# Kernel tuning notes

Measured on AMD Instinct MI355X. Metric: run time of the kernel, lower is better.

## Reference

```python
import jax, jax.numpy as jnp
import numpy as np

IMG = 128                  # img_size
FMM = 35.0
SENSOR = 32.0
FUV = FMM * IMG / SENSOR   # focal length in pixels (screen space, in_ndc=False)
N_PTS = 16384
CHUNK = 1024               # points per scan step
R_SIL = 0.008              # silhouette pass radius (NDC)
R_DEP = 0.012              # depth pass radius (NDC)
K_SIL = 8
K_DEP = 16
DIST = 1.2


def _look_at(dist, elev_deg, azim_deg):
    # PyTorch3D look_at_view_transform with at=origin, up=+Y, degrees=True
    elev = jnp.deg2rad(elev_deg)
    azim = jnp.deg2rad(azim_deg)
    cam = jnp.stack([dist * jnp.cos(elev) * jnp.sin(azim),
                     dist * jnp.sin(elev),
                     dist * jnp.cos(elev) * jnp.cos(azim)], axis=-1)  # (B,3)
    up = jnp.array([0.0, 1.0, 0.0], dtype=cam.dtype)
    z_ax = -cam / (jnp.linalg.norm(cam, axis=-1, keepdims=True) + 1e-8)
    x_ax = jnp.cross(jnp.broadcast_to(up, z_ax.shape), z_ax)
    x_ax = x_ax / (jnp.linalg.norm(x_ax, axis=-1, keepdims=True) + 1e-8)
    y_ax = jnp.cross(z_ax, x_ax)
    R = jnp.stack([x_ax, y_ax, z_ax], axis=-1)   # columns are camera axes
    T = -jnp.einsum('bi,bij->bj', cam, R)        # X_cam = X_world @ R + T
    return R, T


def _project(pts, R, T):
    # world -> camera (row-vector convention) -> screen px -> PyTorch3D NDC
    Xc = jnp.einsum('bni,bij->bnj', pts, R) + T[:, None, :]
    z = Xc[..., 2]
    z_safe = jnp.where(z > 1e-5, z, 1.0)  # points behind camera are culled anyway
    xs = FUV * Xc[..., 0] / z_safe + IMG / 2.0
    ys = FUV * Xc[..., 1] / z_safe + IMG / 2.0
    x_ndc = 1.0 - 2.0 * xs / IMG
    y_ndc = 1.0 - 2.0 * ys / IMG
    return jnp.stack([x_ndc, y_ndc], axis=-1), z


def _rasterize(xy, z, r2, K):
    """Per-pixel K nearest-in-depth points within per-point NDC radius.
    xy: (B,N,2) NDC, z: (B,N) camera depth, r2: (B,N) squared radius.
    Returns zbuf, dists of shape (B,IMG,IMG,K), -1 for empty slots."""
    B, N, _ = xy.shape
    P = IMG * IMG
    # pixel-center NDC grid (PyTorch3D: +X left, +Y up; row-major flatten)
    gxs = 1.0 - (2.0 * jnp.arange(IMG, dtype=xy.dtype) + 1.0) / IMG  # per column
    gys = 1.0 - (2.0 * jnp.arange(IMG, dtype=xy.dtype) + 1.0) / IMG  # per row
    gx = jnp.tile(gxs, IMG)          # (P,)
    gy = jnp.repeat(gys, IMG)        # (P,)

    nch = N // CHUNK
    px = xy[..., 0].reshape(B, nch, CHUNK).swapaxes(0, 1)
    py = xy[..., 1].reshape(B, nch, CHUNK).swapaxes(0, 1)
    pz = z.reshape(B, nch, CHUNK).swapaxes(0, 1)
    pr2 = r2.reshape(B, nch, CHUNK).swapaxes(0, 1)

    def body(carry, c):
        top_z, top_d = carry
        cx, cy, cz, cr2 = c                               # each (B,CHUNK)
        dx = gx[None, :, None] - cx[:, None, :]           # (B,P,CHUNK)
        dy = gy[None, :, None] - cy[:, None, :]
        d2 = dx * dx + dy * dy
        ok = (d2 < cr2[:, None, :]) & (cz[:, None, :] > 0.0)
        zc = jnp.where(ok, cz[:, None, :], jnp.inf)
        cand_z = jnp.concatenate([top_z, zc], axis=-1)    # (B,P,K+CHUNK)
        cand_d = jnp.concatenate([top_d, d2], axis=-1)
        negz, idx = jax.lax.top_k(-cand_z, K)             # K smallest depths
        return (-negz, jnp.take_along_axis(cand_d, idx, axis=-1)), None

    init = (jnp.full((B, P, K), jnp.inf, dtype=xy.dtype),
            jnp.zeros((B, P, K), dtype=xy.dtype))
    (top_z, top_d), _ = jax.lax.scan(jax.checkpoint(body), init, (px, py, pz, pr2))
    valid = jnp.isfinite(top_z)
    zbuf = jnp.where(valid, top_z, -1.0).reshape(B, IMG, IMG, K)
    dists = jnp.where(valid, top_d, -1.0).reshape(B, IMG, IMG, K)
    return zbuf, dists


def setup_inputs() -> dict:
    key = jax.random.key(0)
    k1, k2 = jax.random.split(key)
    point_cloud = jax.random.normal(k1, (2, N_PTS, 6), dtype=jnp.float32) * 0.25
    param = jax.random.normal(k2, (2, 8, 3), dtype=jnp.float32) * 20.0  # degrees
    return {"point_cloud": point_cloud, "param": param}


def reference(point_cloud, param):
    pts = point_cloud[..., :3]
    B = pts.shape[0]
    elev0 = param[:, 1, 0]
    azim0 = param[:, 0, 0]

    # ---- silhouette pass (radius 0.008, K=8) + alpha compositing ----
    R0, T0 = _look_at(DIST, elev0, azim0)
    xy0, z0 = _project(pts, R0, T0)
    r2_sil = jnp.full((B, N_PTS), R_SIL * R_SIL, dtype=pts.dtype)
    _, dists_s = _rasterize(xy0, z0, r2_sil, K_SIL)
    alphas = jnp.where(dists_s >= 0.0, 1.0 - dists_s / (R_SIL * R_SIL), 0.0)
    trans = jnp.cumprod(1.0 - alphas, axis=-1)
    trans_excl = jnp.concatenate([jnp.ones_like(trans[..., :1]), trans[..., :-1]], axis=-1)
    sihlt_map = jnp.sum(alphas * trans_excl, axis=-1, keepdims=True) * 255.0  # (B,H,W,1)

    # ---- depth pass with random view (radius 0.012, K=16) ----
    kd = jax.random.key(42)
    ke, ka = jax.random.split(kd)
    elev_d = jax.random.uniform(ke, (B,), dtype=pts.dtype) * 60.0 - 30.0
    azim_d = jax.random.uniform(ka, (B,), dtype=pts.dtype) * 300.0 + azim0 + 30.0
    Rd, Td = _look_at(DIST, elev_d, azim_d)
    xyd, zd = _project(pts, Rd, Td)
    r2_dep = jnp.full((B, N_PTS), R_DEP * R_DEP, dtype=pts.dtype)
    zbuf_d, _ = _rasterize(xyd, zd, r2_dep, K_DEP)
    depth_ini = zbuf_d[..., 0]

    # density-aware adaptive radius (detached, per source .detach())
    area = jnp.sum((jax.lax.stop_gradient(depth_ini) > 0.0).astype(pts.dtype), axis=(1, 2))
    pa_radius = area / 16384.0 * 0.057                      # (B,)
    r2_ada = jnp.broadcast_to((pa_radius * pa_radius)[:, None], (B, N_PTS))

    zbuf_a, dists_a = _rasterize(xyd, zd, r2_ada, K_DEP)
    depth_img = zbuf_a[..., :8]
    dist_top = dists_a[..., :8]
    return (sihlt_map, depth_img, dist_top)
```

## Files before the change

kernel.cpp:

```cpp
#include <hip/hip_runtime.h>
#include <hip/hip_cooperative_groups.h>
#include <cstring>
#include <cstdint>

namespace cg = cooperative_groups;

#define NPTS 16384
#define FUVC 140.0f
#define R_SILF 0.008f
#define R_DEPF 0.012f
#define R2_SIL (0.008f*0.008f)
#define R2_DEP (0.012f*0.012f)
#define CH 512

#define AREA_OFF  48
#define PA_OFF    50
#define R2ADA_OFF 52
#define TICK0     54
#define TICK1     55
#define CNT_SIL   64
#define OFF_SIL   2112
#define CNT_ADA   4160
#define OFF_ADA   6208
#define FLAGS8    8256
#define FLAGS     8256
#define ZERO_END  16448
#define PROJ0     41024
#define PROJ1     172096
#define LSILF     303168
#define LADAF     827456
#define WS1_WORDS 2007104u
#define WS1_NEEDED ((size_t)WS1_WORDS * 4u)
#define LSIL      303168
#define LADA      434240
#define WS2_WORDS 729152u
#define WS2_NEEDED ((size_t)WS2_WORDS * 4u)

#define FUSED_BLOCKS 1024
#define FUSED_NT (FUSED_BLOCKS * 256)

__device__ __forceinline__ void cam_calc(float elev, float azim, float c[12]) {
    const float D2R = 0.017453292519943295f;
    float er = elev * D2R, ar = azim * D2R;
    float ce = cosf(er), se = sinf(er), ca = cosf(ar), sa = sinf(ar);
    float cx = 1.2f * ce * sa, cy = 1.2f * se, cz = 1.2f * ce * ca;
    float n = sqrtf(cx*cx + cy*cy + cz*cz) + 1e-8f;
    float zx = -cx / n, zy = -cy / n, zz = -cz / n;
    float xx = zz, xy = 0.0f, xz = -zx;
    float xn = sqrtf(xx*xx + xy*xy + xz*xz) + 1e-8f;
    xx /= xn; xz /= xn;
    float yx = zy*xz - zz*xy, yy = zz*xx - zx*xz, yz = zx*xy - zy*xx;
    c[0]=xx; c[1]=xy; c[2]=xz; c[3]=yx; c[4]=yy; c[5]=yz;
    c[6]=zx; c[7]=zy; c[8]=zz;
    c[9]  = -(cx*xx + cy*xy + cz*xz);
    c[10] = -(cx*yx + cy*yy + cz*yz);
    c[11] = -(cx*zx + cy*zy + cz*zz);
}

__device__ __forceinline__ void cam_compute(const float* __restrict__ param,
                                            float* __restrict__ ws,
                                            int t, float ue0, float ue1,
                                            float ua0, float ua1) {
    int b = t >> 1, cam = t & 1;
    float azim0 = param[b * 24 + 0];
    float elev0 = param[b * 24 + 3];
    float elev, azim;
    if (cam == 0) { elev = elev0; azim = azim0; }
    else {
        float ue = b ? ue1 : ue0;
        float ua = b ? ua1 : ua0;
        elev = ue * 60.0f - 30.0f;
        azim = ua * 300.0f + azim0 + 30.0f;
    }
    float c[12];
    cam_calc(elev, azim, c);
    float* w = ws + t * 12;
    #pragma unroll
    for (int i = 0; i < 12; i++) w[i] = c[i];
}

__device__ __forceinline__ float4 project_pt(const float* __restrict__ P,
                                             const float c[12]) {
    float X = P[0], Y = P[1], Z = P[2];
    float xc = X*c[0] + Y*c[1] + Z*c[2] + c[9];
    float yc = X*c[3] + Y*c[4] + Z*c[5] + c[10];
    float zc = X*c[6] + Y*c[7] + Z*c[8] + c[11];
    float zs = zc > 1e-5f ? zc : 1.0f;
    float px = 1.0f - (FUVC * xc / zs + 64.0f) * (1.0f/64.0f);
    float py = 1.0f - (FUVC * yc / zs + 64.0f) * (1.0f/64.0f);
    return make_float4(px, py, zc, 0.0f);
}

// ... 53 lines not shown
        bool take = oz[7 - k] < tz[k];
        mz[k] = take ? oz[7 - k] : tz[k];
        md[k] = take ? od[7 - k] : td[k];
    }
    CE8(0,4) CE8(1,5) CE8(2,6) CE8(3,7)
    CE8(0,2) CE8(1,3) CE8(4,6) CE8(5,7)
    CE8(0,1) CE8(2,3) CE8(4,5) CE8(6,7)
    #pragma unroll
    for (int k = 0; k < 8; k++) { tz[k] = mz[k]; td[k] = md[k]; }
}

__device__ __forceinline__ void merge_seq8(float tz[8], float td[8],
                                           const float* __restrict__ ozp,
                                           const float* __restrict__ odp) {
    float mz[8], md[8];
    #pragma unroll
    for (int k = 0; k < 8; k++) {
        float oz = ozp[7 - k], od = odp[7 - k];
        bool take = oz < tz[k];
        mz[k] = take ? oz : tz[k];
        md[k] = take ? od : td[k];
    }
    CE8(0,4) CE8(1,5) CE8(2,6) CE8(3,7)
    CE8(0,2) CE8(1,3) CE8(4,6) CE8(5,7)
    CE8(0,1) CE8(2,3) CE8(4,5) CE8(6,7)
    #pragma unroll
    for (int k = 0; k < 8; k++) { tz[k] = mz[k]; td[k] = md[k]; }
}

__device__ __forceinline__ void scan1024(unsigned* uw, unsigned cbase,
                                         unsigned obase, unsigned* s, int t) {
    unsigned c0 = uw[cbase + t*4 + 0];
    unsigned c1 = uw[cbase + t*4 + 1];
    unsigned c2 = uw[cbase + t*4 + 2];
    unsigned c3 = uw[cbase + t*4 + 3];
    unsigned tot = c0 + c1 + c2 + c3;
    s[t] = tot; __syncthreads();
    for (int off = 1; off < 256; off <<= 1) {
        unsigned v = (t >= off) ? s[t - off] : 0u;
        __syncthreads();
        s[t] += v;
        __syncthreads();
    }
    unsigned base = s[t] - tot;
    uw[obase + t*4 + 0] = base;
    uw[obase + t*4 + 1] = base + c0;
    uw[obase + t*4 + 2] = base + c0 + c1;
    uw[obase + t*4 + 3] = base + c0 + c1 + c2;
    uw[cbase + t*4 + 0] = 0;
    uw[cbase + t*4 + 1] = 0;
    uw[cbase + t*4 + 2] = 0;
    uw[cbase + t*4 + 3] = 0;
}

__device__ __forceinline__ void body_area_scan(float* __restrict__ ws, int job,
                                               int t, unsigned* s) {
    unsigned* uw = (unsigned*)ws;
    if (job < 2) {
        int b = job;
        unsigned acc = 0;
        #pragma unroll
        for (int j = 0; j < 16; j++) {
            unsigned w = uw[FLAGS8 + b * 4096 + t * 16 + j];
            acc += __popc(w & 0x01010101u);
        }
        s[t] = acc; __syncthreads();
        for (int off = 128; off > 0; off >>= 1) {
            if (t < off) s[t] += s[t + off];
            __syncthreads();
        }
        if (t == 0) {
            unsigned area = s[0];
            uw[AREA_OFF + b] = area;
            float pa = (float)area * (1.0f/16384.0f) * 0.057f;
            ws[PA_OFF + b] = pa;
            ws[R2ADA_OFF + b] = pa * pa;
        }
    } else {
        int b = job - 2;
        scan1024(uw, CNT_SIL + b * 1024, OFF_SIL + b * 1024, s, t);
    }
}

__device__ __forceinline__ void body_cnt_ada(float* __restrict__ ws, int p) {
    unsigned* uw = (unsigned*)ws;
    int b = p >> 14;
    float4 q = ((const float4*)(ws + PROJ1))[p];
    float pa = ws[PA_OFF + b];
    int bxl, bxh, byl, byh;
    bin_bbox(q, pa, bxl, bxh, byl, byh);
    for (int by = byl; by <= byh; by++)
        for (int bx = bxl; bx <= bxh; bx++)
            atomicAdd(&uw[CNT_ADA + b * 1024 + by * 32 + bx], 1u);
}

__device__ __forceinline__ void body_scat_sil(float* __restrict__ ws, int p) {
    unsigned* uw = (unsigned*)ws;
    int b = p >> 14;
    float4 q = ((const float4*)(ws + PROJ0))[p];
    int bxl, bxh, byl, byh;
    bin_bbox(q, R_SILF, bxl, bxh, byl, byh);
    for (int by = byl; by <= byh; by++)
        for (int bx = bxl; bx <= bxh; bx++) {
            unsigned bin = b * 1024 + by * 32 + bx;
            unsigned idx = uw[OFF_SIL + bin] + atomicAdd(&uw[CNT_SIL + bin], 1u);
            ((float4*)(ws + LSILF))[b * 65536 + idx] = q;
// ... 25 lines not shown
    int b = p >> 14;
    float4 q = ((const float4*)(ws + PROJ1))[p];
    float pa = ws[PA_OFF + b];
    int bxl, bxh, byl, byh;
    bin_bbox(q, pa, bxl, bxh, byl, byh);
    for (int by = byl; by <= byh; by++)
        for (int bx = bxl; bx <= bxh; bx++) {
            unsigned bin = b * 1024 + by * 32 + bx;
            unsigned idx = uw[OFF_ADA + bin] + atomicAdd(&uw[CNT_ADA + bin], 1u);
            ((float4*)(ws + LADAF))[b * 147456 + idx] = q;
        }
}

__device__ __forceinline__ void body_gather256(const float* __restrict__ ws,
                                               float* __restrict__ out,
                                               int id, int t,
                                               float* __restrict__ sm) {
    const unsigned* uw = (const unsigned*)ws;
    bool sil = id < 2048;
    int gt = sil ? id : id - 2048;
    int b = gt >> 10;
    int tile = gt & 1023;
    int p = t & 15, seg = t >> 4;
    int bx = tile & 31, by = tile >> 5;
    int col = (bx << 2) + (p & 3), row = (by << 2) + (p >> 2);
    float gx = 1.0f - (float)(2*col + 1) * (1.0f/128.0f);
    float gy = 1.0f - (float)(2*row + 1) * (1.0f/128.0f);
    float r2 = sil ? R2_SIL : ws[R2ADA_OFF + b];
    unsigned start = sil ? uw[OFF_SIL + b * 1024 + tile] : uw[OFF_ADA + b * 1024 + tile];
    unsigned len   = sil ? uw[CNT_SIL + b * 1024 + tile] : uw[CNT_ADA + b * 1024 + tile];
    const float4* lst = sil ? ((const float4*)(ws + LSILF)) + b * 65536 + start
                            : ((const float4*)(ws + LADAF)) + b * 147456 + start;

    float tz[8], td[8];
    #pragma unroll
    for (int k = 0; k < 8; k++) { tz[k] = INFINITY; td[k] = 0.0f; }

    unsigned i = (unsigned)seg;
    while (i + 112 < len) {
        float4 cb[8];
        #pragma unroll
        for (int u = 0; u < 8; u++) cb[u] = lst[i + 16u * (unsigned)u];
        #pragma unroll
        for (int u = 0; u < 8; u++) hit_test(cb[u], gx, gy, r2, tz, td);
        i += 128;
    }
    for (; i < len; i += 16) hit_test(lst[i], gx, gy, r2, tz, td);

    merge_sorted8(tz, td, 16);
    merge_sorted8(tz, td, 32);

    int w = t >> 6;
    if ((t & 63) < 16) {
        float* dst = sm + (w * 16 + p) * 16;
        #pragma unroll
        for (int k = 0; k < 8; k++) { dst[k] = tz[k]; dst[8 + k] = td[k]; }
    }
    __syncthreads();
    if (t < 16) {
        #pragma unroll
        for (int ww = 1; ww < 4; ww++) {
            const float* src = sm + (ww * 16 + p) * 16;
            merge_seq8(tz, td, src, src + 8);
        }
        int pix = (b << 14) + row * 128 + col;
        if (sil) {
            float trans = 1.0f, acc = 0.0f;
            #pragma unroll
            for (int k = 0; k < 8; k++) {
                float a = (tz[k] != INFINITY) ? (1.0f - td[k] / R2_SIL) : 0.0f;
                acc += a * trans;
                trans *= (1.0f - a);
            }
            out[pix] = acc * 255.0f;
        } else {
            float* dep = out + 32768  + (size_t)pix * 8;
            float* dst = out + 294912 + (size_t)pix * 8;
            #pragma unroll
            for (int k = 0; k < 8; k++) {
                bool v = (tz[k] != INFINITY);
                dep[k] = v ? tz[k] : -1.0f;
                dst[k] = v ? td[k] : -1.0f;
            }
        }
    }
}

__device__ __forceinline__ void body_gather(const float* __restrict__ ws,
                                            float* __restrict__ out,
                                            int id, int lane) {
    const unsigned* uw = (const unsigned*)ws;
    bool sil = id < 2048;
    int gt = sil ? id : id - 2048;
    int b = gt >> 10;
    int tile = gt & 1023;
    int p = lane & 15, s = lane >> 4;
    int bx = tile & 31, by = tile >> 5;
    int col = (bx << 2) + (p & 3), row = (by << 2) + (p >> 2);
    float gx = 1.0f - (float)(2*col + 1) * (1.0f/128.0f);
    float gy = 1.0f - (float)(2*row + 1) * (1.0f/128.0f);
    float r2 = sil ? R2_SIL : ws[R2ADA_OFF + b];
    unsigned start = sil ? uw[OFF_SIL + b * 1024 + tile] : uw[OFF_ADA + b * 1024 + tile];
    unsigned len   = sil ? uw[CNT_SIL + b * 1024 + tile] : uw[CNT_ADA + b * 1024 + tile];
    const float4* lst = sil ? ((const float4*)(ws + LSILF)) + b * 65536 + start
                            : ((const float4*)(ws + LADAF)) + b * 147456 + start;

    float tz[8], td[8];
    #pragma unroll
    for (int k = 0; k < 8; k++) { tz[k] = INFINITY; td[k] = 0.0f; }

    unsigned i = (unsigned)s;
    while (i + 28 < len) {
        float4 cb[8];
        #pragma unroll
        for (int u = 0; u < 8; u++) cb[u] = lst[i + 4u * (unsigned)u];
        #pragma unroll
        for (int u = 0; u < 8; u++) hit_test(cb[u], gx, gy, r2, tz, td);
        i += 32;
    }
    for (; i < len; i += 4) hit_test(lst[i], gx, gy, r2, tz, td);

    merge_sorted8(tz, td, 16);
    merge_sorted8(tz, td, 32);

    if (s == 0) {
        int pix = (b << 14) + row * 128 + col;
        if (sil) {
            float trans = 1.0f, acc = 0.0f;
            #pragma unroll
            for (int k = 0; k < 8; k++) {
                float a = (tz[k] != INFINITY) ? (1.0f - td[k] / R2_SIL) : 0.0f;
                acc += a * trans;
                trans *= (1.0f - a);
            }
            out[pix] = acc * 255.0f;
        } else {
            float* dep = out + 32768  + (size_t)pix * 8;
            float* dst = out + 294912 + (size_t)pix * 8;
            #pragma unroll
            for (int k = 0; k < 8; k++) {
                bool v = (tz[k] != INFINITY);
                dep[k] = v ? tz[k] : -1.0f;
                dst[k] = v ? td[k] : -1.0f;
            }
        }
    }
}

__global__ __launch_bounds__(256) void k_fusedp(const float* __restrict__ pc,
                                                const float* __restrict__ param,
                                                float* __restrict__ ws,
                                                float* __restrict__ out,
                                                float ue0, float ue1,
                                                float ua0, float ua1) {
    cg::grid_group grid = cg::this_grid();
    unsigned* uw = (unsigned*)ws;
    __shared__ unsigned sh[2048];
    __shared__ unsigned shLast;
    int t = threadIdx.x;
    int tid = blockIdx.x * 256 + t;

    for (int i = 48 + tid; i < ZERO_END; i += FUSED_NT) uw[i] = 0u;
    if (tid < 4) cam_compute(param, ws, tid, ue0, ue1, ua0, ua1);
    grid.sync();

    if (blockIdx.x < 128) {
        int b = blockIdx.x >> 6;
        int p = ((blockIdx.x & 63) << 8) + t;
        unsigned char* fb = (unsigned char*)(uw + FLAGS8);
        const float* P = pc + ((size_t)b * NPTS + p) * 6;
        float c0[12], c1[12];
        const float* w0 = ws + (b * 2) * 12;
        #pragma unroll
        for (int i = 0; i < 12; i++) { c0[i] = w0[i]; c1[i] = w0[12 + i]; }

        #pragma unroll
        for (int j = 0; j < 4; j++) sh[t * 4 + j] = 0u;
        __syncthreads();

        float4 q0 = project_pt(P, c0);
        ((float4*)(ws + PROJ0))[b * NPTS + p] = q0;
        int bxl, bxh, byl, byh;
        bin_bbox(q0, R_SILF, bxl, bxh, byl, byh);
        for (int by = byl; by <= byh; by++)
            for (int bx = bxl; bx <= bxh; bx++)
                atomicAdd(&sh[by * 32 + bx], 1u);

        float4 q1 = project_pt(P, c1);
        ((float4*)(ws + PROJ1))[b * NPTS + p] = q1;
        if (q1.z > 0.0f) {
            int cl, chh, rl, rh;
            pix_range(q1.x, R_DEPF, cl, chh);
            pix_range(q1.y, R_DEPF, rl, rh);
            for (int rr = rl; rr <= rh; rr++) {
                float gyv = 1.0f - (float)(2 * rr + 1) * (1.0f/128.0f);
                float dy = gyv - q1.y;
                for (int cc = cl; cc <= chh; cc++) {
                    float gxv = 1.0f - (float)(2 * cc + 1) * (1.0f/128.0f);
                    float dx = gxv - q1.x;
                    if (dx*dx + dy*dy < R2_DEP) fb[b * NPTS + rr * 128 + cc] = 1;
                }
            }
        }
        __syncthreads();
        #pragma unroll
        for (int j = 0; j < 4; j++) {
            unsigned c = sh[t * 4 + j];
            if (c) atomicAdd(&uw[CNT_SIL + b * 1024 + t * 4 + j], c);
        }
        __threadfence();
    }
    if (t == 0) shLast = (atomicAdd(&uw[TICK0], 1u) == FUSED_BLOCKS - 1) ? 1u : 0u;
    __syncthreads();
    if (shLast) {
        __threadfence();
        for (int job = 0; job < 4; job++) {
            body_area_scan(ws, job, t, sh);
            __syncthreads();
        }
        __threadfence();
    }
    grid.sync();

    if (blockIdx.x < 128) {
        int b = blockIdx.x >> 6;
        int p = ((blockIdx.x & 63) << 8) + t;
        float4 q = ((const float4*)(ws + PROJ1))[b * NPTS + p];
        float pa = ws[PA_OFF + b];
        #pragma unroll
        for (int j = 0; j < 4; j++) sh[t * 4 + j] = 0u;
        __syncthreads();
        int bxl, bxh, byl, byh;
        bin_bbox(q, pa, bxl, bxh, byl, byh);
        for (int by = byl; by <= byh; by++)
            for (int bx = bxl; bx <= bxh; bx++)
                atomicAdd(&sh[by * 32 + bx], 1u);
        __syncthreads();
        #pragma unroll
        for (int j = 0; j < 4; j++) {
            unsigned c = sh[t * 4 + j];
            if (c) atomicAdd(&uw[CNT_ADA + b * 1024 + t * 4 + j], c);
        }
        __threadfence();
    } else if (blockIdx.x < 256) {
        int blk = blockIdx.x - 128;
        int b = blk >> 6;
        int p = ((blk & 63) << 8) + t;
        float4 q = ((const float4*)(ws + PROJ0))[b * NPTS + p];
        int bxl, bxh, byl, byh;
        bin_bbox(q, R_SILF, bxl, bxh, byl, byh);
        #pragma unroll
        for (int j = 0; j < 4; j++) sh[t * 4 + j] = 0u;
        __syncthreads();
        for (int by = byl; by <= byh; by++)
            for (int bx = bxl; bx <= bxh; bx++)
                atomicAdd(&sh[by * 32 + bx], 1u);
        __syncthreads();
        #pragma unroll
        for (int j = 0; j < 4; j++) {
            int bin = t * 4 + j;
            unsigned c = sh[bin];
            unsigned gb = 0;
            if (c) gb = uw[OFF_SIL + b * 1024 + bin] +
                        atomicAdd(&uw[CNT_SIL + b * 1024 + bin], c);
            sh[1024 + bin] = gb;
            sh[bin] = 0u;
        }
        __syncthreads();
        for (int by = byl; by <= byh; by++)
            for (int bx = bxl; bx <= bxh; bx++) {
                int bin = by * 32 + bx;
                unsigned loc = atomicAdd(&sh[bin], 1u);
                ((float4*)(ws + LSILF))[b * 65536 + sh[1024 + bin] + loc] = q;
            }
        __threadfence();
    }
    if (t == 0) shLast = (atomicAdd(&uw[TICK1], 1u) == FUSED_BLOCKS - 1) ? 1u : 0u;
    __syncthreads();
    if (shLast) {
        __threadfence();
        if (t < 128) body_scan_ada(ws, t >> 6, t & 63);
        __threadfence();
    }
    grid.sync();

    if (blockIdx.x < 128) {
        int b = blockIdx.x >> 6;
        int p = ((blockIdx.x & 63) << 8) + t;
        float4 q = ((const float4*)(ws + PROJ1))[b * NPTS + p];
        float pa = ws[PA_OFF + b];
        int bxl, bxh, byl, byh;
        bin_bbox(q, pa, bxl, bxh, byl, byh);
        #pragma unroll
        for (int j = 0; j < 4; j++) sh[t * 4 + j] = 0u;
        __syncthreads();
        for (int by = byl; by <= byh; by++)
            for (int bx = bxl; bx <= bxh; bx++)
                atomicAdd(&sh[by * 32 + bx], 1u);
        __syncthreads();
        #pragma unroll
        for (int j = 0; j < 4; j++) {
            int bin = t * 4 + j;
            unsigned c = sh[bin];
            unsigned gb = 0;
            if (c) gb = uw[OFF_ADA + b * 1024 + bin] +
                        atomicAdd(&uw[CNT_ADA + b * 1024 + bin], c);
            sh[1024 + bin] = gb;
            sh[bin] = 0u;
        }
        __syncthreads();
        for (int by = byl; by <= byh; by++)
            for (int bx = bxl; bx <= bxh; bx++) {
                int bin = by * 32 + bx;
                unsigned loc = atomicAdd(&sh[bin], 1u);
                ((float4*)(ws + LADAF))[b * 147456 + sh[1024 + bin] + loc] = q;
            }
    }
    grid.sync();

    for (int rep = 0; rep < 4; rep++) {
        int id = rep * 1024 + blockIdx.x;
        body_gather256(ws, out, id, t, (float*)sh);
        __syncthreads();
    }
}


__global__ __launch_bounds__(256) void k_zero(float* __restrict__ ws) {
    unsigned* uw = (unsigned*)ws;
    int gid = blockIdx.x * 256 + threadIdx.x;
    int stride = gridDim.x * 256;
    for (int i = 48 + gid; i < ZERO_END; i += stride) uw[i] = 0u;
}

__global__ __launch_bounds__(256) void k_proj_v3(const float* __restrict__ pc,
                                                 const float* __restrict__ param,
                                                 float* __restrict__ ws,
                                                 float ue0, float ue1,
                                                 float ua0, float ua1) {
    int b = blockIdx.x >> 6;
    int p = ((blockIdx.x & 63) << 8) + threadIdx.x;
    float azim0 = param[b * 24 + 0];
    float elev0 = param[b * 24 + 3];
    float c0[12], c1[12];
    cam_calc(elev0, azim0, c0);
    float ue = b ? ue1 : ue0;
    float ua = b ? ua1 : ua0;
    cam_calc(ue * 60.0f - 30.0f, ua * 300.0f + azim0 + 30.0f, c1);

    unsigned* uw = (unsigned*)ws;
    unsigned char* fb = (unsigned char*)(uw + FLAGS8);
    const float* P = pc + ((size_t)b * NPTS + p) * 6;

    float4 q0 = project_pt(P, c0);
    ((float4*)(ws + PROJ0))[b * NPTS + p] = q0;
    int bxl, bxh, byl, byh;
    bin_bbox(q0, R_SILF, bxl, bxh, byl, byh);
    for (int by = byl; by <= byh; by++)
        for (int bx = bxl; bx <= bxh; bx++)
            atomicAdd(&uw[CNT_SIL + b * 1024 + by * 32 + bx], 1u);

    float4 q1 = project_pt(P, c1);
    ((float4*)(ws + PROJ1))[b * NPTS + p] = q1;
    if (q1.z > 0.0f) {
        int cl, chh, rl, rh;
        pix_range(q1.x, R_DEPF, cl, chh);
        pix_range(q1.y, R_DEPF, rl, rh);
        for (int rr = rl; rr <= rh; rr++) {
            float gy = 1.0f - (float)(2 * rr + 1) * (1.0f/128.0f);
            float dy = gy - q1.y;
            for (int cc = cl; cc <= chh; cc++) {
                float gx = 1.0f - (float)(2 * cc + 1) * (1.0f/128.0f);
                float dx = gx - q1.x;
                if (dx*dx + dy*dy < R2_DEP) fb[b * NPTS + rr * 128 + cc] = 1;
            }
        }
    }
}

__global__ __launch_bounds__(256) void k_area_scan_v3(float* __restrict__ ws) {
    __shared__ unsigned s[256];
    body_area_scan(ws, blockIdx.x, threadIdx.x, s);
}

__global__ __launch_bounds__(64) void k_cntada_scatsil(float* __restrict__ ws) {
    int id = blockIdx.x;
    bool isCnt = id < 512;
    int p = ((isCnt ? id : id - 512) << 6) + threadIdx.x;
    if (isCnt) body_cnt_ada(ws, p);
    else       body_scat_sil(ws, p);
}

__global__ __launch_bounds__(64) void k_scan_ada64(float* __restrict__ ws) {
    body_scan_ada(ws, blockIdx.x, threadIdx.x);
}

__global__ __launch_bounds__(64) void k_scatter_ada_v2(float* __restrict__ ws) {
    body_scat_ada(ws, (blockIdx.x << 6) + threadIdx.x);
}

__global__ __launch_bounds__(256) void k_gather_v4(const float* __restrict__ ws,
                                                   float* __restrict__ out) {
    __shared__ float sm[1024];
    body_gather256(ws, out, blockIdx.x, threadIdx.x, sm);
}


__global__ __launch_bounds__(256) void k_init(const float* __restrict__ param,
                                              float* __restrict__ ws,
                                              float ue0, float ue1,
                                              float ua0, float ua1) {
    unsigned* uw = (unsigned*)ws;
    int gid = blockIdx.x * 256 + threadIdx.x;
    int stride = gridDim.x * 256;
    for (int i = gid; i < 2048; i += stride) { uw[CNT_SIL + i] = 0u; uw[CNT_ADA + i] = 0u; }
    for (int i = gid; i < 32768; i += stride) uw[FLAGS + i] = 0u;
    if (gid < 2) uw[AREA_OFF + gid] = 0u;
    if (gid < 4) cam_compute(param, ws, gid, ue0, ue1, ua0, ua1);
}

__global__ __launch_bounds__(256) void k_proj_count(const float* __restrict__ pc,
                                                    float* __restrict__ ws) {
    unsigned* uw = (unsigned*)ws;
    int b = blockIdx.x >> 6;
    int p = ((blockIdx.x & 63) << 8) + threadIdx.x;
    const float* P = pc + ((size_t)b * NPTS + p) * 6;
    float c0[12], c1[12];
    const float* w0 = ws + (b * 2) * 12;
    #pragma unroll
    for (int i = 0; i < 12; i++) { c0[i] = w0[i]; c1[i] = w0[12 + i]; }

    float4 q0 = project_pt(P, c0);
    ((float4*)(ws + PROJ0))[b * NPTS + p] = q0;
    int bxl, bxh, byl, byh;
    bin_bbox(q0, R_SILF, bxl, bxh, byl, byh);
    for (int by = byl; by <= byh; by++)
        for (int bx = bxl; bx <= bxh; bx++)
            atomicAdd(&uw[CNT_SIL + b * 1024 + by * 32 + bx], 1u);

    float4 q1 = project_pt(P, c1);
    ((float4*)(ws + PROJ1))[b * NPTS + p] = q1;
    if (q1.z > 0.0f) {
        int cl, chh, rl, rh;
        pix_range(q1.x, R_DEPF, cl, chh);
        pix_range(q1.y, R_DEPF, rl, rh);
        for (int rr = rl; rr <= rh; rr++) {
            float gy = 1.0f - (float)(2 * rr + 1) * (1.0f/128.0f);
            float dy = gy - q1.y;
            for (int cc = cl; cc <= chh; cc++) {
                float gx = 1.0f - (float)(2 * cc + 1) * (1.0f/128.0f);
                float dx = gx - q1.x;
                if (dx*dx + dy*dy < R2_DEP) uw[FLAGS + b * NPTS + rr * 128 + cc] = 1u;
            }
        }
    }
}
// ... 236 lines not shown
    #pragma unroll
    for (int k = 0; k < 8; k++) {
        bool v = (tz[k] != INFINITY);
        dep[k] = v ? tz[k] : -1.0f;
        dst[k] = v ? td[k] : -1.0f;
    }
}

static inline uint32_t rotl32(uint32_t x, int r) { return (x << r) | (x >> (32 - r)); }

static void tf2x32(uint32_t k0, uint32_t k1, uint32_t c0, uint32_t c1,
                   uint32_t* o0, uint32_t* o1) {
    uint32_t ks0 = k0, ks1 = k1, ks2 = k0 ^ k1 ^ 0x1BD11BDAu;
    uint32_t x0 = c0 + ks0, x1 = c1 + ks1;
    static const int rA[4] = {13, 15, 26, 6};
    static const int rB[4] = {17, 29, 16, 24};
    #define RND4(R) do { for (int i = 0; i < 4; i++) { x0 += x1; x1 = rotl32(x1, R[i]); x1 ^= x0; } } while (0)
    RND4(rA); x0 += ks1; x1 += ks2 + 1u;
    RND4(rB); x0 += ks2; x1 += ks0 + 2u;
    RND4(rA); x0 += ks0; x1 += ks1 + 3u;
    RND4(rB); x0 += ks1; x1 += ks2 + 4u;
    RND4(rA); x0 += ks2; x1 += ks0 + 5u;
    #undef RND4
    *o0 = x0; *o1 = x1;
}

static inline float bits_to_unit_float(uint32_t bits) {
    uint32_t fb = (bits >> 9) | 0x3f800000u;
    float f;
    memcpy(&f, &fb, 4);
    return f - 1.0f;
}

extern "C" void kernel_launch(void* const* d_in, const int* in_sizes, int n_in,
                              void* d_out, int out_size, void* d_ws, size_t ws_size,
                              hipStream_t stream) {
    const float* pc    = (const float*)d_in[0];
    const float* param = (const float*)d_in[1];
    float* out = (float*)d_out;
    float* ws  = (float*)d_ws;

    uint32_t ke0, ke1, ka0, ka1, b1, b2;
    tf2x32(0u, 42u, 0u, 0u, &ke0, &ke1);
    tf2x32(0u, 42u, 0u, 1u, &ka0, &ka1);
    float ue[2], ua[2];
    for (uint32_t i = 0; i < 2; i++) {
        tf2x32(ke0, ke1, 0u, i, &b1, &b2);
        ue[i] = bits_to_unit_float(b1 ^ b2);
        tf2x32(ka0, ka1, 0u, i, &b1, &b2);
        ua[i] = bits_to_unit_float(b1 ^ b2);
    }
    float ue0 = ue[0], ue1 = ue[1], ua0 = ua[0], ua1 = ua[1];

    if (ws_size >= WS1_NEEDED) {
        int dev = 0;
        hipGetDevice(&dev);
        hipDeviceProp_t prop;
        bool coop = (hipGetDeviceProperties(&prop, dev) == hipSuccess) &&
                    prop.cooperativeLaunch;
        if (coop) {
            int maxB = 0;
            if (hipOccupancyMaxActiveBlocksPerMultiprocessor(&maxB, k_fusedp, 256, 0)
                    != hipSuccess ||
                maxB * prop.multiProcessorCount < FUSED_BLOCKS)
                coop = false;
        }
        if (coop) {
            void* args[] = { (void*)&pc, (void*)&param, (void*)&ws, (void*)&out,
                             (void*)&ue0, (void*)&ue1, (void*)&ua0, (void*)&ua1 };
            hipError_t e = hipLaunchCooperativeKernel((const void*)k_fusedp,
                                                      dim3(FUSED_BLOCKS), dim3(256),
                                                      args, 0, stream);
            if (e == hipSuccess) return;
        }
        k_zero          <<<16, 256, 0, stream>>>(ws);
        k_proj_v3       <<<128, 256, 0, stream>>>(pc, param, ws, ue0, ue1, ua0, ua1);
        k_area_scan_v3  <<<4, 256, 0, stream>>>(ws);
        k_cntada_scatsil<<<1024, 64, 0, stream>>>(ws);
        k_scan_ada64    <<<2, 64, 0, stream>>>(ws);
        k_scatter_ada_v2<<<512, 64, 0, stream>>>(ws);
        k_gather_v4     <<<4096, 256, 0, stream>>>(ws, out);
    } else if (ws_size >= WS2_NEEDED) {
        k_init      <<<64, 256, 0, stream>>>(param, ws, ue0, ue1, ua0, ua1);
        k_proj_count<<<128, 256, 0, stream>>>(pc, ws);
        k_area_scan <<<4, 256, 0, stream>>>(ws);
        k_count_ada <<<128, 256, 0, stream>>>(ws);
        k_scan_ada  <<<2, 256, 0, stream>>>(ws);
        k_scatter   <<<128, 256, 0, stream>>>(ws);
        k_gather_sil<<<128, 256, 0, stream>>>(ws, out);
        k_gather_ada<<<128, 256, 0, stream>>>(ws, out);
    } else {
        cam_kernel_fb<<<1, 64, 0, stream>>>(param, ws, ue0, ue1, ua0, ua1);
        raster_AB<<<256, 256, 0, stream>>>(pc, ws, out);
        raster_C <<<128, 256, 0, stream>>>(pc, ws, out);
    }
}
```

Measured before the change: 85.72 us.

## Restructure cooperative kernel to three grid syncs with per-block histograms

Replaces the cooperative fused kernel with a version that drops the initial zeroing and camera grid sync. Each block computes its camera inline and writes non-atomic per-block histograms and coverage bitmaps to workspace, and the adaptive list is binned by a conservative maximum radius so its counts can be computed before the area is known. Separate blocks then perform reductions and scans, which removes the last-block ticket logic and one full counting pass. The change needs more workspace, and the larger adaptive bins add candidate points to the gather. Shared-memory merge rows are padded to 17 floats to avoid bank conflicts.

```diff
diff --git a/kernel.cpp b/kernel.cpp
--- a/kernel.cpp
+++ b/kernel.cpp
@@ -9,6 +9,7 @@
 #define FUVC 140.0f
 #define R_SILF 0.008f
 #define R_DEPF 0.012f
+#define R_ADA_MAXF 0.057f
 #define R2_SIL (0.008f*0.008f)
 #define R2_DEP (0.012f*0.012f)
 #define CH 512
@@ -16,8 +17,6 @@
 #define AREA_OFF  48
 #define PA_OFF    50
 #define R2ADA_OFF 52
-#define TICK0     54
-#define TICK1     55
 #define CNT_SIL   64
 #define OFF_SIL   2112
 #define CNT_ADA   4160
@@ -35,9 +34,17 @@
 #define LADA      434240
 #define WS2_WORDS 729152u
 #define WS2_NEEDED ((size_t)WS2_WORDS * 4u)
+#define HSIL      2007104u
+#define HADA      2138176u
+#define BMAP      2269248u
+#define OFFA_SIL  2334784u
+#define OFFB_SIL  2336834u
+#define OFFA_ADA  2338882u
+#define OFFB_ADA  2340932u
+#define WS0_WORDS 2342980u
+#define WS0_NEEDED ((size_t)WS0_WORDS * 4u)
 
 #define FUSED_BLOCKS 1024
-#define FUSED_NT (FUSED_BLOCKS * 256)
 
 __device__ __forceinline__ void cam_calc(float elev, float azim, float c[12]) {
     const float D2R = 0.017453292519943295f;
@@ -197,6 +204,297 @@
     uw[cbase + t*4 + 2] = 0;
     uw[cbase + t*4 + 3] = 0;
 }
+
+__device__ __forceinline__ void job_scan64(unsigned* __restrict__ uw,
+                                           unsigned histBase, unsigned offaBase,
+                                           unsigned offbBase, unsigned* s, int t) {
+    unsigned c[4];
+    #pragma unroll
+    for (int j = 0; j < 4; j++) {
+        int bin = t * 4 + j;
+        unsigned acc = 0;
+        for (int blk = 0; blk < 64; blk++)
+            acc += uw[histBase + blk * 1024 + bin];
+        c[j] = acc;
+    }
+    unsigned tot = c[0] + c[1] + c[2] + c[3];
+    s[t] = tot; __syncthreads();
+    for (int off = 1; off < 256; off <<= 1) {
+        unsigned v = (t >= off) ? s[t - off] : 0u;
+        __syncthreads();
+        s[t] += v;
+        __syncthreads();
+    }
+    unsigned run = s[t] - tot;
+    #pragma unroll
+    for (int j = 0; j < 4; j++) {
+        uw[offaBase + t * 4 + j] = run;
+        uw[offbBase + t * 4 + j] = run;
+        run += c[j];
+    }
+    if (t == 255) uw[offaBase + 1024] = s[255];
+}
+
+__device__ __forceinline__ void job_area64(float* __restrict__ ws,
+                                           unsigned bmapBase, int b,
+                                           unsigned* s, int t) {
+    unsigned* uw = (unsigned*)ws;
+    unsigned acc = 0;
+    #pragma unroll
+    for (int w = 0; w < 2; w++) {
+        int word = t * 2 + w;
+        unsigned orv = 0;
+        for (int blk = 0; blk < 64; blk++)
+            orv |= uw[bmapBase + blk * 512 + word];
+        acc += __popc(orv);
+    }
+    s[t] = acc; __syncthreads();
+    for (int off = 128; off > 0; off >>= 1) {
+        if (t < off) s[t] += s[t + off];
+        __syncthreads();
+    }
+    if (t == 0) {
+        float pa = (float)s[0] * (1.0f/16384.0f) * 0.057f;
+        ws[R2ADA_OFF + b] = pa * pa;
+    }
+}
+
+__device__ __forceinline__ void body_gather256v2(const float* __restrict__ ws,
+                                                 float* __restrict__ out,
+                                                 int id, int t,
+                                                 float* __restrict__ sm) {
+    const unsigned* uw = (const unsigned*)ws;
+    bool sil = id < 2048;
+    int gt = sil ? id : id - 2048;
+    int b = gt >> 10;
+    int tile = gt & 1023;
+    int p = t & 15, seg = t >> 4;
+    int bx = tile & 31, by = tile >> 5;
+    int col = (bx << 2) + (p & 3), row = (by << 2) + (p >> 2);
+    float gx = 1.0f - (float)(2*col + 1) * (1.0f/128.0f);
+    float gy = 1.0f - (float)(2*row + 1) * (1.0f/128.0f);
+    float r2 = sil ? R2_SIL : ws[R2ADA_OFF + b];
+    unsigned offa = sil ? (OFFA_SIL + b * 1025 + tile) : (OFFA_ADA + b * 1025 + tile);
+    unsigned start = uw[offa];
+    unsigned len   = uw[offa + 1] - start;
+    const float4* lst = sil ? ((const float4*)(ws + LSILF)) + b * 65536 + start
+                            : ((const float4*)(ws + LADAF)) + b * 147456 + start;
+
+    float tz[8], td[8];
+    #pragma unroll
+    for (int k = 0; k < 8; k++) { tz[k] = INFINITY; td[k] = 0.0f; }
+
+    unsigned i = (unsigned)seg;
+    while (i + 112 < len) {
+        float4 cb[8];
+        #pragma unroll
+        for (int u = 0; u < 8; u++) cb[u] = lst[i + 16u * (unsigned)u];
+        #pragma unroll
+        for (int u = 0; u < 8; u++) hit_test(cb[u], gx, gy, r2, tz, td);
+        i += 128;
+    }
+    for (; i < len; i += 16) hit_test(lst[i], gx, gy, r2, tz, td);
+
+    merge_sorted8(tz, td, 16);
+    merge_sorted8(tz, td, 32);
+
+    int w = t >> 6;
+    if ((t & 63) < 16) {
+        float* dst = sm + (w * 16 + p) * 17;
+        #pragma unroll
+        for (int k = 0; k < 8; k++) { dst[k] = tz[k]; dst[8 + k] = td[k]; }
+    }
+    __syncthreads();
+    if (t < 16) {
+        #pragma unroll
+        for (int ww = 1; ww < 4; ww++) {
+            const float* src = sm + (ww * 16 + p) * 17;
+            merge_seq8(tz, td, src, src + 8);
+        }
+        int pix = (b << 14) + row * 128 + col;
+        if (sil) {
+            float trans = 1.0f, acc = 0.0f;
+            #pragma unroll
+            for (int k = 0; k < 8; k++) {
+                float a = (tz[k] != INFINITY) ? (1.0f - td[k] / R2_SIL) : 0.0f;
+                acc += a * trans;
+                trans *= (1.0f - a);
+            }
+            out[pix] = acc * 255.0f;
+        } else {
+            float* dep = out + 32768  + (size_t)pix * 8;
+            float* dst = out + 294912 + (size_t)pix * 8;
+            #pragma unroll
+            for (int k = 0; k < 8; k++) {
+                bool v = (tz[k] != INFINITY);
+                dep[k] = v ? tz[k] : -1.0f;
+                dst[k] = v ? td[k] : -1.0f;
+            }
+        }
+    }
+}
+
+__global__ __launch_bounds__(256) void k_fused3(const float* __restrict__ pc,
+                                                const float* __restrict__ param,
+                                                float* __restrict__ ws,
+                                                float* __restrict__ out,
+                                                float ue0, float ue1,
+                                                float ua0, float ua1) {
+    cg::grid_group grid = cg::this_grid();
+    unsigned* uw = (unsigned*)ws;
+    __shared__ unsigned sh[2048];
+    int t = threadIdx.x;
+    int blk = blockIdx.x;
+
+    if (blk < 128) {
+        int b = blk >> 6;
+        int p = ((blk & 63) << 8) + t;
+        float azim0 = param[b * 24 + 0];
+        float elev0 = param[b * 24 + 3];
+        float c0[12];
+        cam_calc(elev0, azim0, c0);
+        #pragma unroll
+        for (int j = 0; j < 4; j++) sh[t * 4 + j] = 0u;
+        __syncthreads();
+        float4 q0 = project_pt(pc + ((size_t)b * NPTS + p) * 6, c0);
+        ((float4*)(ws + PROJ0))[b * NPTS + p] = q0;
+        int bxl, bxh, byl, byh;
+        bin_bbox(q0, R_SILF, bxl, bxh, byl, byh);
+        for (int by = byl; by <= byh; by++)
+            for (int bx = bxl; bx <= bxh; bx++)
+                atomicAdd(&sh[by * 32 + bx], 1u);
+        __syncthreads();
+        #pragma unroll
+        for (int j = 0; j < 4; j++)
+            uw[HSIL + blk * 1024 + t * 4 + j] = sh[t * 4 + j];
+    } else if (blk < 256) {
+        int blk2 = blk - 128;
+        int b = blk2 >> 6;
+        int p = ((blk2 & 63) << 8) + t;
+        float azim0 = param[b * 24 + 0];
+        float ue = b ? ue1 : ue0;
+        float ua = b ? ua1 : ua0;
+        float c1[12];
+        cam_calc(ue * 60.0f - 30.0f, ua * 300.0f + azim0 + 30.0f, c1);
+        #pragma unroll
+        for (int j = 0; j < 4; j++) sh[t * 4 + j] = 0u;
+        sh[1024 + t * 2 + 0] = 0u;
+        sh[1024 + t * 2 + 1] = 0u;
+        __syncthreads();
+        float4 q1 = project_pt(pc + ((size_t)b * NPTS + p) * 6, c1);
+        ((float4*)(ws + PROJ1))[b * NPTS + p] = q1;
+        if (q1.z > 0.0f) {
+            int cl, chh, rl, rh;
+            pix_range(q1.x, R_DEPF, cl, chh);
+            pix_range(q1.y, R_DEPF, rl, rh);
+            for (int rr = rl; rr <= rh; rr++) {
+                float gyv = 1.0f - (float)(2 * rr + 1) * (1.0f/128.0f);
+                float dy = gyv - q1.y;
+                for (int cc = cl; cc <= chh; cc++) {
+                    float gxv = 1.0f - (float)(2 * cc + 1) * (1.0f/128.0f);
+                    float dx = gxv - q1.x;
+                    if (dx*dx + dy*dy < R2_DEP) {
+                        int pix = rr * 128 + cc;
+                        atomicOr(&sh[1024 + (pix >> 5)], 1u << (pix & 31));
+                    }
+                }
+            }
+        }
+        int bxl, bxh, byl, byh;
+        bin_bbox(q1, R_ADA_MAXF, bxl, bxh, byl, byh);
+        for (int by = byl; by <= byh; by++)
+            for (int bx = bxl; bx <= bxh; bx++)
+                atomicAdd(&sh[by * 32 + bx], 1u);
+        __syncthreads();
+        #pragma unroll
+        for (int j = 0; j < 4; j++)
+            uw[HADA + blk2 * 1024 + t * 4 + j] = sh[t * 4 + j];
+        uw[BMAP + blk2 * 512 + t * 2 + 0] = sh[1024 + t * 2 + 0];
+        uw[BMAP + blk2 * 512 + t * 2 + 1] = sh[1024 + t * 2 + 1];
+    }
+    grid.sync();
+
+    if (blk < 2) {
+        job_scan64(uw, HSIL + blk * 65536, OFFA_SIL + blk * 1025,
+                   OFFB_SIL + blk * 1024, sh, t);
+    } else if (blk < 4) {
+        int b = blk - 2;
+        job_scan64(uw, HADA + b * 65536, OFFA_ADA + b * 1025,
+                   OFFB_ADA + b * 1024, sh, t);
+    } else if (blk < 6) {
+        int b = blk - 4;
+        job_area64(ws, BMAP + b * 32768, b, sh, t);
+    }
+    grid.sync();
+
+    if (blk < 128) {
+        int b = blk >> 6;
+        int p = ((blk & 63) << 8) + t;
+        float4 q = ((const float4*)(ws + PROJ0))[b * NPTS + p];
+        int bxl, bxh, byl, byh;
+        bin_bbox(q, R_SILF, bxl, bxh, byl, byh);
+        #pragma unroll
+        for (int j = 0; j < 4; j++) sh[t * 4 + j] = 0u;
+        __syncthreads();
+        for (int by = byl; by <= byh; by++)
+            for (int bx = bxl; bx <= bxh; bx++)
+                atomicAdd(&sh[by * 32 + bx], 1u);
+        __syncthreads();
+        #pragma unroll
+        for (int j = 0; j < 4; j++) {
+            int bin = t * 4 + j;
+            unsigned c = sh[bin];
+            unsigned gb = 0;
+            if (c) gb = atomicAdd(&uw[OFFB_SIL + b * 1024 + bin], c);
+            sh[1024 + bin] = gb;
+            sh[bin] = 0u;
+        }
+        __syncthreads();
+        for (int by = byl; by <= byh; by++)
+            for (int bx = bxl; bx <= bxh; bx++) {
+                int bin = by * 32 + bx;
+                unsigned loc = atomicAdd(&sh[bin], 1u);
+                ((float4*)(ws + LSILF))[b * 65536 + sh[1024 + bin] + loc] = q;
+            }
+    } else if (blk < 256) {
+        int blk2 = blk - 128;
+        int b = blk2 >> 6;
+        int p = ((blk2 & 63) << 8) + t;
+        float4 q = ((const float4*)(ws + PROJ1))[b * NPTS + p];
+        int bxl, bxh, byl, byh;
+        bin_bbox(q, R_ADA_MAXF, bxl, bxh, byl, byh);
+        #pragma unroll
+        for (int j = 0; j < 4; j++) sh[t * 4 + j] = 0u;
+        __syncthreads();
+        for (int by = byl; by <= byh; by++)
+            for (int bx = bxl; bx <= bxh; bx++)
+                atomicAdd(&sh[by * 32 + bx], 1u);
+        __syncthreads();
+        #pragma unroll
+        for (int j = 0; j < 4; j++) {
+            int bin = t * 4 + j;
+            unsigned c = sh[bin];
+            unsigned gb = 0;
+            if (c) gb = atomicAdd(&uw[OFFB_ADA + b * 1024 + bin], c);
+            sh[1024 + bin] = gb;
+            sh[bin] = 0u;
+        }
+        __syncthreads();
+        for (int by = byl; by <= byh; by++)
+            for (int bx = bxl; bx <= bxh; bx++) {
+                int bin = by * 32 + bx;
+                unsigned loc = atomicAdd(&sh[bin], 1u);
+                ((float4*)(ws + LADAF))[b * 147456 + sh[1024 + bin] + loc] = q;
+            }
+    }
+    grid.sync();
+
+    for (int rep = 0; rep < 4; rep++) {
+        body_gather256v2(ws, out, rep * 1024 + blk, t, (float*)sh);
+        __syncthreads();
+    }
+}
+
 
 __device__ __forceinline__ void body_area_scan(float* __restrict__ ws, int job,
                                                int t, unsigned* s) {
@@ -328,7 +626,7 @@
 
     int w = t >> 6;
     if ((t & 63) < 16) {
-        float* dst = sm + (w * 16 + p) * 16;
+        float* dst = sm + (w * 16 + p) * 17;
         #pragma unroll
         for (int k = 0; k < 8; k++) { dst[k] = tz[k]; dst[8 + k] = td[k]; }
     }
@@ -336,7 +634,7 @@
     if (t < 16) {
         #pragma unroll
         for (int ww = 1; ww < 4; ww++) {
-            const float* src = sm + (ww * 16 + p) * 16;
+            const float* src = sm + (ww * 16 + p) * 17;
             merge_seq8(tz, td, src, src + 8);
         }
         int pix = (b << 14) + row * 128 + col;
@@ -362,246 +660,6 @@
     }
 }
 
-__device__ __forceinline__ void body_gather(const float* __restrict__ ws,
-                                            float* __restrict__ out,
-                                            int id, int lane) {
-    const unsigned* uw = (const unsigned*)ws;
-    bool sil = id < 2048;
-    int gt = sil ? id : id - 2048;
-    int b = gt >> 10;
-    int tile = gt & 1023;
-    int p = lane & 15, s = lane >> 4;
-    int bx = tile & 31, by = tile >> 5;
-    int col = (bx << 2) + (p & 3), row = (by << 2) + (p >> 2);
-    float gx = 1.0f - (float)(2*col + 1) * (1.0f/128.0f);
-    float gy = 1.0f - (float)(2*row + 1) * (1.0f/128.0f);
-    float r2 = sil ? R2_SIL : ws[R2ADA_OFF + b];
-    unsigned start = sil ? uw[OFF_SIL + b * 1024 + tile] : uw[OFF_ADA + b * 1024 + tile];
-    unsigned len   = sil ? uw[CNT_SIL + b * 1024 + tile] : uw[CNT_ADA + b * 1024 + tile];
-    const float4* lst = sil ? ((const float4*)(ws + LSILF)) + b * 65536 + start
-                            : ((const float4*)(ws + LADAF)) + b * 147456 + start;
-
-    float tz[8], td[8];
-    #pragma unroll
-    for (int k = 0; k < 8; k++) { tz[k] = INFINITY; td[k] = 0.0f; }
-
-    unsigned i = (unsigned)s;
-    while (i + 28 < len) {
-        float4 cb[8];
-        #pragma unroll
-        for (int u = 0; u < 8; u++) cb[u] = lst[i + 4u * (unsigned)u];
-        #pragma unroll
-        for (int u = 0; u < 8; u++) hit_test(cb[u], gx, gy, r2, tz, td);
-        i += 32;
-    }
-    for (; i < len; i += 4) hit_test(lst[i], gx, gy, r2, tz, td);
-
-    merge_sorted8(tz, td, 16);
-    merge_sorted8(tz, td, 32);
-
-    if (s == 0) {
-        int pix = (b << 14) + row * 128 + col;
-        if (sil) {
-            float trans = 1.0f, acc = 0.0f;
-            #pragma unroll
-            for (int k = 0; k < 8; k++) {
-                float a = (tz[k] != INFINITY) ? (1.0f - td[k] / R2_SIL) : 0.0f;
-                acc += a * trans;
-                trans *= (1.0f - a);
-            }
-            out[pix] = acc * 255.0f;
-        } else {
-            float* dep = out + 32768  + (size_t)pix * 8;
-            float* dst = out + 294912 + (size_t)pix * 8;
-            #pragma unroll
-            for (int k = 0; k < 8; k++) {
-                bool v = (tz[k] != INFINITY);
-                dep[k] = v ? tz[k] : -1.0f;
-                dst[k] = v ? td[k] : -1.0f;
-            }
-        }
-    }
-}
-
-__global__ __launch_bounds__(256) void k_fusedp(const float* __restrict__ pc,
-                                                const float* __restrict__ param,
-                                                float* __restrict__ ws,
-                                                float* __restrict__ out,
-                                                float ue0, float ue1,
-                                                float ua0, float ua1) {
-    cg::grid_group grid = cg::this_grid();
-    unsigned* uw = (unsigned*)ws;
-    __shared__ unsigned sh[2048];
-    __shared__ unsigned shLast;
-    int t = threadIdx.x;
-    int tid = blockIdx.x * 256 + t;
-
-    for (int i = 48 + tid; i < ZERO_END; i += FUSED_NT) uw[i] = 0u;
-    if (tid < 4) cam_compute(param, ws, tid, ue0, ue1, ua0, ua1);
-    grid.sync();
-
-    if (blockIdx.x < 128) {
-        int b = blockIdx.x >> 6;
-        int p = ((blockIdx.x & 63) << 8) + t;
-        unsigned char* fb = (unsigned char*)(uw + FLAGS8);
-        const float* P = pc + ((size_t)b * NPTS + p) * 6;
-        float c0[12], c1[12];
-        const float* w0 = ws + (b * 2) * 12;
-        #pragma unroll
-        for (int i = 0; i < 12; i++) { c0[i] = w0[i]; c1[i] = w0[12 + i]; }
-
-        #pragma unroll
-        for (int j = 0; j < 4; j++) sh[t * 4 + j] = 0u;
-        __syncthreads();
-
-        float4 q0 = project_pt(P, c0);
-        ((float4*)(ws + PROJ0))[b * NPTS + p] = q0;
-        int bxl, bxh, byl, byh;
-        bin_bbox(q0, R_SILF, bxl, bxh, byl, byh);
-        for (int by = byl; by <= byh; by++)
-            for (int bx = bxl; bx <= bxh; bx++)
-                atomicAdd(&sh[by * 32 + bx], 1u);
-
-        float4 q1 = project_pt(P, c1);
-        ((float4*)(ws + PROJ1))[b * NPTS + p] = q1;
-        if (q1.z > 0.0f) {
-            int cl, chh, rl, rh;
-            pix_range(q1.x, R_DEPF, cl, chh);
-            pix_range(q1.y, R_DEPF, rl, rh);
-            for (int rr = rl; rr <= rh; rr++) {
-                float gyv = 1.0f - (float)(2 * rr + 1) * (1.0f/128.0f);
-                float dy = gyv - q1.y;
-                for (int cc = cl; cc <= chh; cc++) {
-                    float gxv = 1.0f - (float)(2 * cc + 1) * (1.0f/128.0f);
-                    float dx = gxv - q1.x;
-                    if (dx*dx + dy*dy < R2_DEP) fb[b * NPTS + rr * 128 + cc] = 1;
-                }
-            }
-        }
-        __syncthreads();
-        #pragma unroll
-        for (int j = 0; j < 4; j++) {
-            unsigned c = sh[t * 4 + j];
-            if (c) atomicAdd(&uw[CNT_SIL + b * 1024 + t * 4 + j], c);
-        }
-        __threadfence();
-    }
-    if (t == 0) shLast = (atomicAdd(&uw[TICK0], 1u) == FUSED_BLOCKS - 1) ? 1u : 0u;
-    __syncthreads();
-    if (shLast) {
-        __threadfence();
-        for (int job = 0; job < 4; job++) {
-            body_area_scan(ws, job, t, sh);
-            __syncthreads();
-        }
-        __threadfence();
-    }
-    grid.sync();
-
-    if (blockIdx.x < 128) {
-        int b = blockIdx.x >> 6;
-        int p = ((blockIdx.x & 63) << 8) + t;
-        float4 q = ((const float4*)(ws + PROJ1))[b * NPTS + p];
-        float pa = ws[PA_OFF + b];
-        #pragma unroll
-        for (int j = 0; j < 4; j++) sh[t * 4 + j] = 0u;
-        __syncthreads();
-        int bxl, bxh, byl, byh;
-        bin_bbox(q, pa, bxl, bxh, byl, byh);
-        for (int by = byl; by <= byh; by++)
-            for (int bx = bxl; bx <= bxh; bx++)
-                atomicAdd(&sh[by * 32 + bx], 1u);
-        __syncthreads();
-        #pragma unroll
-        for (int j = 0; j < 4; j++) {
-            unsigned c = sh[t * 4 + j];
-            if (c) atomicAdd(&uw[CNT_ADA + b * 1024 + t * 4 + j], c);
-        }
-        __threadfence();
-    } else if (blockIdx.x < 256) {
-        int blk = blockIdx.x - 128;
-        int b = blk >> 6;
-        int p = ((blk & 63) << 8) + t;
-        float4 q = ((const float4*)(ws + PROJ0))[b * NPTS + p];
-        int bxl, bxh, byl, byh;
-        bin_bbox(q, R_SILF, bxl, bxh, byl, byh);
-        #pragma unroll
-        for (int j = 0; j < 4; j++) sh[t * 4 + j] = 0u;
-        __syncthreads();
-        for (int by = byl; by <= byh; by++)
-            for (int bx = bxl; bx <= bxh; bx++)
-                atomicAdd(&sh[by * 32 + bx], 1u);
-        __syncthreads();
-        #pragma unroll
-        for (int j = 0; j < 4; j++) {
-            int bin = t * 4 + j;
-            unsigned c = sh[bin];
-            unsigned gb = 0;
-            if (c) gb = uw[OFF_SIL + b * 1024 + bin] +
-                        atomicAdd(&uw[CNT_SIL + b * 1024 + bin], c);
-            sh[1024 + bin] = gb;
-            sh[bin] = 0u;
-        }
-        __syncthreads();
-        for (int by = byl; by <= byh; by++)
-            for (int bx = bxl; bx <= bxh; bx++) {
-                int bin = by * 32 + bx;
-                unsigned loc = atomicAdd(&sh[bin], 1u);
-                ((float4*)(ws + LSILF))[b * 65536 + sh[1024 + bin] + loc] = q;
-            }
-        __threadfence();
-    }
-    if (t == 0) shLast = (atomicAdd(&uw[TICK1], 1u) == FUSED_BLOCKS - 1) ? 1u : 0u;
-    __syncthreads();
-    if (shLast) {
-        __threadfence();
-        if (t < 128) body_scan_ada(ws, t >> 6, t & 63);
-        __threadfence();
-    }
-    grid.sync();
-
-    if (blockIdx.x < 128) {
-        int b = blockIdx.x >> 6;
-        int p = ((blockIdx.x & 63) << 8) + t;
-        float4 q = ((const float4*)(ws + PROJ1))[b * NPTS + p];
-        float pa = ws[PA_OFF + b];
-        int bxl, bxh, byl, byh;
-        bin_bbox(q, pa, bxl, bxh, byl, byh);
-        #pragma unroll
-        for (int j = 0; j < 4; j++) sh[t * 4 + j] = 0u;
-        __syncthreads();
-        for (int by = byl; by <= byh; by++)
-            for (int bx = bxl; bx <= bxh; bx++)
-                atomicAdd(&sh[by * 32 + bx], 1u);
-        __syncthreads();
-        #pragma unroll
-        for (int j = 0; j < 4; j++) {
-            int bin = t * 4 + j;
-            unsigned c = sh[bin];
-            unsigned gb = 0;
-            if (c) gb = uw[OFF_ADA + b * 1024 + bin] +
-                        atomicAdd(&uw[CNT_ADA + b * 1024 + bin], c);
-            sh[1024 + bin] = gb;
-            sh[bin] = 0u;
-        }
-        __syncthreads();
-        for (int by = byl; by <= byh; by++)
-            for (int bx = bxl; bx <= bxh; bx++) {
-                int bin = by * 32 + bx;
-                unsigned loc = atomicAdd(&sh[bin], 1u);
-                ((float4*)(ws + LADAF))[b * 147456 + sh[1024 + bin] + loc] = q;
-            }
-    }
-    grid.sync();
-
-    for (int rep = 0; rep < 4; rep++) {
-        int id = rep * 1024 + blockIdx.x;
-        body_gather256(ws, out, id, t, (float*)sh);
-        __syncthreads();
-    }
-}
-
-
 __global__ __launch_bounds__(256) void k_zero(float* __restrict__ ws) {
     unsigned* uw = (unsigned*)ws;
     int gid = blockIdx.x * 256 + threadIdx.x;
@@ -677,7 +735,7 @@
 
 __global__ __launch_bounds__(256) void k_gather_v4(const float* __restrict__ ws,
                                                    float* __restrict__ out) {
-    __shared__ float sm[1024];
+    __shared__ float sm[1088];
     body_gather256(ws, out, blockIdx.x, threadIdx.x, sm);
 }
 
@@ -1020,7 +1078,7 @@
     }
     float ue0 = ue[0], ue1 = ue[1], ua0 = ua[0], ua1 = ua[1];
 
-    if (ws_size >= WS1_NEEDED) {
+    if (ws_size >= WS0_NEEDED) {
         int dev = 0;
         hipGetDevice(&dev);
         hipDeviceProp_t prop;
@@ -1028,7 +1086,7 @@
                     prop.cooperativeLaunch;
         if (coop) {
             int maxB = 0;
-            if (hipOccupancyMaxActiveBlocksPerMultiprocessor(&maxB, k_fusedp, 256, 0)
+            if (hipOccupancyMaxActiveBlocksPerMultiprocessor(&maxB, k_fused3, 256, 0)
                     != hipSuccess ||
                 maxB * prop.multiProcessorCount < FUSED_BLOCKS)
                 coop = false;
@@ -1036,11 +1094,13 @@
         if (coop) {
             void* args[] = { (void*)&pc, (void*)&param, (void*)&ws, (void*)&out,
                              (void*)&ue0, (void*)&ue1, (void*)&ua0, (void*)&ua1 };
-            hipError_t e = hipLaunchCooperativeKernel((const void*)k_fusedp,
+            hipError_t e = hipLaunchCooperativeKernel((const void*)k_fused3,
                                                       dim3(FUSED_BLOCKS), dim3(256),
                                                       args, 0, stream);
             if (e == hipSuccess) return;
         }
+    }
+    if (ws_size >= WS1_NEEDED) {
         k_zero          <<<16, 256, 0, stream>>>(ws);
         k_proj_v3       <<<128, 256, 0, stream>>>(pc, param, ws, ue0, ue1, ua0, ua1);
         k_area_scan_v3  <<<4, 256, 0, stream>>>(ws);
```

New measurement: 85.91 us. No clear change (+0.2%).
